# Kernel optimization log

Measured on AMD Instinct MI355X. Metric: run time of the kernel, lower is better.

## Reference

```python
import jax, jax.numpy as jnp
import numpy as np

EPS = 1e-6

def _layernorm(x, gamma, beta):
    mu = jnp.mean(x, axis=-1, keepdims=True)
    var = jnp.mean(jnp.square(x - mu), axis=-1, keepdims=True)
    return (x - mu) * jax.lax.rsqrt(var + EPS) * gamma + beta


def setup_inputs() -> dict:
    key = jax.random.key(0)
    ks = jax.random.split(key, 8)
    B, N, C, F = 2, 2048, 1024, 4096
    s = 0.02
    return {
        "x": jax.random.normal(ks[0], (B, N, C), jnp.float32),
        "Wq": jax.random.normal(ks[1], (C, C), jnp.float32) * s,
        "Wk": jax.random.normal(ks[2], (C, C), jnp.float32) * s,
        "Wv": jax.random.normal(ks[3], (C, C), jnp.float32) * s,
        "Wp": jax.random.normal(ks[4], (C, C), jnp.float32) * s,
        "bp": jnp.zeros((C,), jnp.float32),
        "W1": jax.random.normal(ks[5], (C, F), jnp.float32) * s,
        "b1": jnp.zeros((F,), jnp.float32),
        "W2": jax.random.normal(ks[6], (F, C), jnp.float32) * s,
        "b2": jnp.zeros((C,), jnp.float32),
        "gamma1": jnp.ones((C,), jnp.float32),
        "beta1": jnp.zeros((C,), jnp.float32),
        "gamma2": jnp.ones((C,), jnp.float32),
        "beta2": jnp.zeros((C,), jnp.float32),
    }


def reference(x, Wq, Wk, Wv, Wp, bp, W1, b1, W2, b2, gamma1, beta1, gamma2, beta2):
    B, N, C = x.shape
    H = 16
    D = C // H
    scale = D ** -0.5

    xn = _layernorm(x, gamma1, beta1)
    # QKV projections (no bias); q pre-scaled by head_dim**-0.5 as in source
    q = (xn @ Wq * scale).reshape(B, N, H, D).transpose(0, 2, 1, 3)  # bhnd
    k = (xn @ Wk).reshape(B, N, H, D).transpose(0, 2, 1, 3)
    v = (xn @ Wv).reshape(B, N, H, D).transpose(0, 2, 1, 3)

    attn = jax.nn.softmax(jnp.einsum("bhnd,bhmd->bhnm", q, k), axis=-1)
    y = jnp.einsum("bhnm,bhmd->bhnd", attn, v)
    y = y.transpose(0, 2, 1, 3).reshape(B, N, C)
    x = x + (y @ Wp + bp)

    xn2 = _layernorm(x, gamma2, beta2)
    h = jax.nn.gelu(xn2 @ W1 + b1, approximate=False)  # keras 'gelu' is exact
    x = x + (h @ W2 + b2)
    return x
```

## Files before the change

### kernel.cpp

```cpp
#include <hip/hip_runtime.h>
#include <math.h>

#define BN  4096
#define SEQ 2048
#define CH  1024
#define FF  4096
#define NH  16
#define HD  64

typedef short bf16x8 __attribute__((ext_vector_type(8)));
typedef float f32x4  __attribute__((ext_vector_type(4)));

#define MFMA16(a,b,c) __builtin_amdgcn_mfma_f32_16x16x32_bf16(a,b,c,0,0,0)

__device__ __forceinline__ unsigned short f2b(float f){
  unsigned u = __float_as_uint(f);
  u += 0x7fffu + ((u>>16)&1u);
  return (unsigned short)(u>>16);
}

__device__ __forceinline__ unsigned pk2(float a, float b){
  return __builtin_amdgcn_perm(__float_as_uint(b), __float_as_uint(a), 0x07060302u);
}

#if __has_builtin(__builtin_amdgcn_exp2f)
__device__ __forceinline__ float fexp2(float x){ return __builtin_amdgcn_exp2f(x); }
#else
__device__ __forceinline__ float fexp2(float x){
  float r; asm("v_exp_f32 %0, %1" : "=v"(r) : "v"(x)); return r;
}
#endif

__device__ __forceinline__ void gl2lds16(const void* g, void* l){
  __builtin_amdgcn_global_load_lds(
      (__attribute__((address_space(1))) void*)g,
      (__attribute__((address_space(3))) void*)l, 16, 0, 0);
}

__global__ __launch_bounds__(256) void transpose_all(
    const float* __restrict__ Wq, const float* __restrict__ Wk,
    const float* __restrict__ Wv, const float* __restrict__ Wp,
    const float* __restrict__ W1, const float* __restrict__ W2,
    unsigned short* __restrict__ wq_t, unsigned short* __restrict__ wk_t,
    unsigned short* __restrict__ wv_t, unsigned short* __restrict__ wp_t,
    unsigned short* __restrict__ w1_t, unsigned short* __restrict__ w2_t)
{
  const int id = blockIdx.x;
  const float* in; unsigned short* out; int R, S, bx, by; float scale = 1.f;
  if (id < 1024){
    const int which = id >> 8, sub = id & 255;
    R = CH; S = CH; bx = sub & 15; by = sub >> 4;
    if (which == 0){ in = Wq; out = wq_t; scale = 0.18033688011112042f; }
    else if (which == 1){ in = Wk; out = wk_t; }
    else if (which == 2){ in = Wv; out = wv_t; }
    else               { in = Wp; out = wp_t; }
  } else if (id < 2048){
    const int sub = id - 1024; in = W1; out = w1_t; R = CH; S = FF;
    bx = sub & 63; by = sub >> 6;
  } else {
    const int sub = id - 2048; in = W2; out = w2_t; R = FF; S = CH;
    bx = sub & 15; by = sub >> 4;
  }
  __shared__ float tile[64][65];
  const int tid = threadIdx.x;
  const int tx = tid & 63, ty = tid >> 6;
  const int s0 = bx * 64, r0 = by * 64;
  #pragma unroll
  for (int j = 0; j < 16; j++){
    int r = ty + j*4;
    tile[r][tx] = in[(size_t)(r0 + r)*S + s0 + tx];
  }
  __syncthreads();
  #pragma unroll
  for (int j = 0; j < 16; j++){
    int s = ty + j*4;
    out[(size_t)(s0 + s)*R + r0 + tx] = f2b(tile[tx][s] * scale);
  }
}

__global__ __launch_bounds__(256) void ln_kernel(const float* __restrict__ x,
    const float* __restrict__ gamma, const float* __restrict__ beta,
    unsigned short* __restrict__ out)
{
  const int row = blockIdx.x, tid = threadIdx.x;
  const float4 xv = ((const float4*)(x + (size_t)row*CH))[tid];
  float s  = xv.x + xv.y + xv.z + xv.w;
  float ss = xv.x*xv.x + xv.y*xv.y + xv.z*xv.z + xv.w*xv.w;
  #pragma unroll
  for (int off = 1; off < 64; off <<= 1){
    s  += __shfl_xor(s,  off, 64);
    ss += __shfl_xor(ss, off, 64);
  }
  __shared__ float red[8];
  const int w = tid >> 6;
  if ((tid & 63) == 0){ red[w] = s; red[4+w] = ss; }
  __syncthreads();
  s  = red[0]+red[1]+red[2]+red[3];
  ss = red[4]+red[5]+red[6]+red[7];
  const float mu   = s * (1.f/CH);
  const float rstd = rsqrtf(ss*(1.f/CH) - mu*mu + 1e-6f);
  const float4 g = ((const float4*)gamma)[tid];
  const float4 b = ((const float4*)beta )[tid];
  ushort4 o;
  o.x = f2b((xv.x-mu)*rstd*g.x + b.x);
  o.y = f2b((xv.y-mu)*rstd*g.y + b.y);
  o.z = f2b((xv.z-mu)*rstd*g.z + b.z);
  o.w = f2b((xv.w-mu)*rstd*g.w + b.w);
  ((ushort4*)(out + (size_t)row*CH))[tid] = o;
}

template<int BNT,int BIAS,int GELU,int RES,int OMODE,int SPLITK>
__global__ __launch_bounds__(256,2) void gemm_bt(const unsigned short* __restrict__ A,
    const unsigned short* __restrict__ Bt, const float* __restrict__ bias,
    const float* __restrict__ resid, float* __restrict__ outF,
    unsigned short* __restrict__ outB, unsigned short* __restrict__ outK,
    unsigned short* __restrict__ outV, int M, int Nn, int K)
{
  constexpr int MI = (BNT==128) ? 4 : 2;
  constexpr int BCH = (BNT==128) ? 4 : 2;
  __shared__ __align__(16) unsigned short Al[128*64];
  __shared__ __align__(16) unsigned short Bl[BNT*64];
  const int tid = threadIdx.x;
  const int w = tid >> 6, lane = tid & 63;
  const int quad = lane >> 4, l16 = lane & 15;
  const int m0 = blockIdx.y*128, n0 = blockIdx.x*BNT;
  const int wm = (BNT==128) ? (w >> 1)*64 : w*32;
  const int wn = (BNT==128) ? (w & 1)*64 : 0;
  const int srow = lane >> 3, sslot = lane & 7;
  f32x4 acc[MI][4] = {};
  const int kseg = SPLITK > 1 ? K / SPLITK : K;
  const int kBeg = SPLITK > 1 ? blockIdx.z * kseg : 0;
  for (int k0 = kBeg; k0 < kBeg + kseg; k0 += 64){
    __syncthreads();
    #pragma unroll
    for (int i = 0; i < 4; i++){
      const int rb = (w*4 + i)*8;
      const int r = rb + srow;
      const int c = sslot ^ (r & 7);
      gl2lds16(A + (size_t)(m0 + r)*K + k0 + c*8, (char*)Al + rb*128);
    }
    #pragma unroll
    for (int i = 0; i < BCH; i++){
      const int rb = (w*BCH + i)*8;
      const int r = rb + srow;
      const int c = sslot ^ (r & 7);
      gl2lds16(Bt + (size_t)(n0 + r)*K + k0 + c*8, (char*)Bl + rb*128);
    }
    __syncthreads();
    #pragma unroll
    for (int kc = 0; kc < 2; kc++){
      bf16x8 af[MI], bfr[4];
      #pragma unroll
      for (int mi = 0; mi < MI; mi++){
        const int r = wm + mi*16 + l16;
        af[mi] = *(const bf16x8*)(Al + r*64 + (((kc*4 + quad) ^ (r & 7))*8));
      }
      #pragma unroll
      for (int nj = 0; nj < 4; nj++){
        const int r = wn + nj*16 + l16;
        bfr[nj] = *(const bf16x8*)(Bl + r*64 + (((kc*4 + quad) ^ (r & 7))*8));
      }
      #pragma unroll
      for (int mi = 0; mi < MI; mi++)
        #pragma unroll
        for (int nj = 0; nj < 4; nj++)
          acc[mi][nj] = MFMA16(af[mi], bfr[nj], acc[mi][nj]);
    }
  }
  #pragma unroll
  for (int nj = 0; nj < 4; nj++){
    const int col = n0 + wn + nj*16 + l16;
    const float bv = BIAS ? bias[col] : 0.f;
    #pragma unroll
    for (int mi = 0; mi < MI; mi++){
      #pragma unroll
      for (int r = 0; r < 4; r++){
        const int row = m0 + wm + mi*16 + quad*4 + r;
        float v = acc[mi][nj][r];
        if (SPLITK > 1){
          if (blockIdx.z == 0){
            if (BIAS) v += bias[col];
            if (RES)  v += resid[(size_t)row*Nn + col];
          }
          atomicAdd(&outF[(size_t)row*Nn + col], v);
          continue;
        }
        v += bv;
        if (GELU) v = 0.5f*v*(1.f + erff(v*0.70710678118654752f));
        if (RES)  v += resid[(size_t)row*Nn + col];
        if (OMODE == 0) outF[(size_t)row*Nn + col] = v;
        else if (OMODE == 1) outB[(size_t)row*Nn + col] = f2b(v);
        else {
          const int cg = col >> 10, c = col & (CH-1);
          if (cg == 0)      outB[(size_t)row*CH + c] = f2b(v);
          else if (cg == 1) outK[(size_t)row*CH + c] = f2b(v);
          else {
            const int bb = row >> 11, n = row & (SEQ-1);
            const int hh = c >> 6,  d = c & (HD-1);
            const int np = (n & ~63) | (((n & 15) << 2) | ((n >> 4) & 3));
            outV[((size_t)((bb*NH + hh)*HD + d))*SEQ + np] = f2b(v);
          }
        }
      }
    }
  }
}

__global__ __launch_bounds__(256,2) void attn_kernel(const unsigned short* __restrict__ q,
    const unsigned short* __restrict__ k, const unsigned short* __restrict__ vt,
    unsigned short* __restrict__ y)
{
  __shared__ __align__(16) unsigned short Kl[2][64*64];
  __shared__ __align__(16) unsigned short Vl[2][64*64];
  __shared__ __align__(16) unsigned short Pp[4][64*68];
  const int tid = threadIdx.x;
  const int w = tid >> 6, lane = tid & 63;
  const int wq = w & 1, wk = w >> 1;
  const int quad = lane >> 4, l16 = lane & 15;
  const int bh = blockIdx.y;
  const int b = bh >> 4, h = bh & 15;
  const size_t tb  = ((size_t)b*SEQ)*CH + h*HD;
  const size_t vb_ = (size_t)bh*HD*SEQ;
  const int qr0 = blockIdx.x*128 + wq*64;

  bf16x8 qf[4][2];
  #pragma unroll
  for (int mi = 0; mi < 4; mi++)
    #pragma unroll
    for (int kc = 0; kc < 2; kc++)
      qf[mi][kc] = *(const bf16x8*)(q + tb + (size_t)(qr0 + mi*16 + l16)*CH + kc*32 + quad*8);

  float sacc[4][4];
  f32x4 o[4][4] = {};
  #pragma unroll
  for (int mi = 0; mi < 4; mi++)
    #pragma unroll
    for (int r = 0; r < 4; r++) sacc[mi][r] = 0.f;

  for (int t = 0; t < 16; t++){
    const int kv0 = wk*1024 + t*64;
    __syncthreads();
    #pragma unroll
    for (int i = 0; i < 8; i++){
      const int r = i*8 + (lane >> 3);
      const int c = (lane & 7) ^ (r & 7);
      if (wq == 0)
        gl2lds16(k  + tb  + (size_t)(kv0 + r)*CH + c*8, (char*)&Kl[wk][0] + i*1024);
      else
        gl2lds16(vt + vb_ + (size_t)r*SEQ + kv0 + c*8, (char*)&Vl[wk][0] + i*1024);
    }
    __syncthreads();

    f32x4 s[4][4] = {};
    #pragma unroll
    for (int kc = 0; kc < 2; kc++){
      #pragma unroll
      for (int nj = 0; nj < 4; nj++){
        bf16x8 kf = *(const bf16x8*)(&Kl[wk][0] + (nj*16 + l16)*64 + (((kc*4 + quad) ^ (l16 & 7))*8));
        #pragma unroll
        for (int mi = 0; mi < 4; mi++)
          s[mi][nj] = MFMA16(qf[mi][kc], kf, s[mi][nj]);
      }
    }
    #pragma unroll
    for (int mi = 0; mi < 4; mi++){
      #pragma unroll
      for (int r = 0; r < 4; r++){
        const float p0 = fexp2(s[mi][0][r]);
        const float p1 = fexp2(s[mi][1][r]);
        const float p2 = fexp2(s[mi][2][r]);
        const float p3 = fexp2(s[mi][3][r]);
        sacc[mi][r] += (p0 + p1) + (p2 + p3);
        uint2 pk;
        pk.x = pk2(p0, p1);
        pk.y = pk2(p2, p3);
        const int prow = mi*16 + quad*4 + r;
        *(uint2*)(&Pp[w][prow*68 + l16*4]) = pk;
      }
    }
    #pragma unroll
    for (int kc = 0; kc < 2; kc++){
      bf16x8 pa[4];
      #pragma unroll
      for (int mi = 0; mi < 4; mi++)
        pa[mi] = *(const bf16x8*)(&Pp[w][(mi*16 + l16)*68 + kc*32 + quad*8]);
      #pragma unroll
      for (int nd = 0; nd < 4; nd++){
        bf16x8 vf = *(const bf16x8*)(&Vl[wk][0] + (nd*16 + l16)*64 + (((kc*4 + quad) ^ (l16 & 7))*8));
        #pragma unroll
        for (int mi = 0; mi < 4; mi++)
          o[mi][nd] = MFMA16(pa[mi], vf, o[mi][nd]);
      }
    }
  }

  __syncthreads();
  float* ob = wq ? (float*)&Vl[0][0] : (float*)&Kl[0][0];
  float* sb = (float*)&Pp[2 + wq][0];
  if (wk == 1){
    #pragma unroll
    for (int mi = 0; mi < 4; mi++)
      #pragma unroll
      for (int nd = 0; nd < 4; nd++)
        #pragma unroll
        for (int r = 0; r < 4; r++){
          const int idx = (mi*4 + nd)*4 + r;
          ob[lane*64 + ((idx + lane) & 63)] = o[mi][nd][r];
        }
    #pragma unroll
    for (int mi = 0; mi < 4; mi++)
      #pragma unroll
      for (int r = 0; r < 4; r++)
        sb[lane*16 + ((mi*4 + r + lane) & 15)] = sacc[mi][r];
  }
  __syncthreads();
  if (wk == 0){
    #pragma unroll
    for (int mi = 0; mi < 4; mi++)
      #pragma unroll
      for (int nd = 0; nd < 4; nd++)
        #pragma unroll
        for (int r = 0; r < 4; r++){
          const int idx = (mi*4 + nd)*4 + r;
          o[mi][nd][r] += ob[lane*64 + ((idx + lane) & 63)];
        }
    #pragma unroll
    for (int mi = 0; mi < 4; mi++){
      #pragma unroll
      for (int r = 0; r < 4; r++){
        float sum = sacc[mi][r] + sb[lane*16 + ((mi*4 + r + lane) & 15)];
        #pragma unroll
        for (int off = 1; off < 16; off <<= 1) sum += __shfl_xor(sum, off, 64);
        const float inv = 1.f / sum;
        const int qr = qr0 + mi*16 + quad*4 + r;
        #pragma unroll
        for (int nd = 0; nd < 4; nd++)
          y[tb + (size_t)qr*CH + nd*16 + l16] = f2b(o[mi][nd][r]*inv);
      }
    }
  }
}

extern "C" void kernel_launch(void* const* d_in, const int* in_sizes, int n_in,
                              void* d_out, int out_size, void* d_ws, size_t ws_size,
                              hipStream_t stream)
{
  (void)in_sizes; (void)n_in; (void)out_size; (void)ws_size;
  const float* x   = (const float*)d_in[0];
  const float* Wq  = (const float*)d_in[1];
  const float* Wk  = (const float*)d_in[2];
  const float* Wv  = (const float*)d_in[3];
  const float* Wp  = (const float*)d_in[4];
  const float* bp  = (const float*)d_in[5];
  const float* W1  = (const float*)d_in[6];
  const float* b1  = (const float*)d_in[7];
  const float* W2  = (const float*)d_in[8];
  const float* b2  = (const float*)d_in[9];
  const float* g1  = (const float*)d_in[10];
  const float* be1 = (const float*)d_in[11];
  const float* g2  = (const float*)d_in[12];
  const float* be2 = (const float*)d_in[13];
  float* out = (float*)d_out;
  char* ws = (char*)d_ws;
  const size_t MB = 1024*1024;
  unsigned short* wq_t = (unsigned short*)(ws +  0*MB);
  unsigned short* wk_t = (unsigned short*)(ws +  2*MB);
  unsigned short* wv_t = (unsigned short*)(ws +  4*MB);
  unsigned short* wp_t = (unsigned short*)(ws +  6*MB);
  unsigned short* w1_t = (unsigned short*)(ws +  8*MB);
  unsigned short* w2_t = (unsigned short*)(ws + 16*MB);
  unsigned short* xn   = (unsigned short*)(ws + 24*MB);
  unsigned short* qb   = (unsigned short*)(ws + 32*MB);
  unsigned short* kb   = (unsigned short*)(ws + 40*MB);
  unsigned short* vtb  = (unsigned short*)(ws + 48*MB);
  unsigned short* yb   = (unsigned short*)(ws + 56*MB);
  float*          x2   = (float*)         (ws + 64*MB);
  unsigned short* xn2  = (unsigned short*)(ws + 80*MB);
  unsigned short* hb   = (unsigned short*)(ws + 88*MB);

  transpose_all<<<3072,256,0,stream>>>(Wq, Wk, Wv, Wp, W1, W2,
                                       wq_t, wk_t, wv_t, wp_t, w1_t, w2_t);

  ln_kernel<<<BN,256,0,stream>>>(x, g1, be1, xn);
  gemm_bt<128,0,0,0,3,0><<<dim3(24,32),256,0,stream>>>(xn, wq_t, nullptr, nullptr,
      nullptr, qb, kb, vtb, BN, 3072, CH);
  attn_kernel<<<dim3(16,32),256,0,stream>>>(qb, kb, vtb, yb);
  gemm_bt<64,1,0,1,0,0><<<dim3(16,32),256,0,stream>>>(yb, wp_t, bp, x, x2,
      nullptr, nullptr, nullptr, BN, CH, CH);
  ln_kernel<<<BN,256,0,stream>>>(x2, g2, be2, xn2);
  gemm_bt<128,1,1,0,1,0><<<dim3(32,32),256,0,stream>>>(xn2, w1_t, b1, nullptr, nullptr,
      hb, nullptr, nullptr, BN, FF, CH);
  hipMemsetAsync(out, 0, (size_t)BN*CH*sizeof(float), stream);
  gemm_bt<128,1,0,1,0,4><<<dim3(8,32,4),256,0,stream>>>(hb, w2_t, b2, x2, out,
      nullptr, nullptr, nullptr, BN, CH, FF);
}
```

Before: 381.1 us.

## Fuse LayerNorm into weight-prep kernel, shrink attention P buffer, retune W2 GEMM

```diff
diff --git a/kernel.cpp b/kernel.cpp
--- a/kernel.cpp
+++ b/kernel.cpp
@@ -37,7 +37,9 @@
       (__attribute__((address_space(3))) void*)l, 16, 0, 0);
 }
 
-__global__ __launch_bounds__(256) void transpose_all(
+__global__ __launch_bounds__(256) void prep_kernel(
+    const float* __restrict__ x, const float* __restrict__ g1,
+    const float* __restrict__ be1, unsigned short* __restrict__ xn,
     const float* __restrict__ Wq, const float* __restrict__ Wk,
     const float* __restrict__ Wv, const float* __restrict__ Wp,
     const float* __restrict__ W1, const float* __restrict__ W2,
@@ -46,6 +48,35 @@
     unsigned short* __restrict__ w1_t, unsigned short* __restrict__ w2_t)
 {
   const int id = blockIdx.x;
+  const int tid = threadIdx.x;
+  if (id >= 3072){
+    const int row = id - 3072;
+    const float4 xv = ((const float4*)(x + (size_t)row*CH))[tid];
+    float s  = xv.x + xv.y + xv.z + xv.w;
+    float ss = xv.x*xv.x + xv.y*xv.y + xv.z*xv.z + xv.w*xv.w;
+    #pragma unroll
+    for (int off = 1; off < 64; off <<= 1){
+      s  += __shfl_xor(s,  off, 64);
+      ss += __shfl_xor(ss, off, 64);
+    }
+    __shared__ float red[8];
+    const int w = tid >> 6;
+    if ((tid & 63) == 0){ red[w] = s; red[4+w] = ss; }
+    __syncthreads();
+    s  = red[0]+red[1]+red[2]+red[3];
+    ss = red[4]+red[5]+red[6]+red[7];
+    const float mu   = s * (1.f/CH);
+    const float rstd = rsqrtf(ss*(1.f/CH) - mu*mu + 1e-6f);
+    const float4 g = ((const float4*)g1)[tid];
+    const float4 b = ((const float4*)be1)[tid];
+    ushort4 o;
+    o.x = f2b((xv.x-mu)*rstd*g.x + b.x);
+    o.y = f2b((xv.y-mu)*rstd*g.y + b.y);
+    o.z = f2b((xv.z-mu)*rstd*g.z + b.z);
+    o.w = f2b((xv.w-mu)*rstd*g.w + b.w);
+    ((ushort4*)(xn + (size_t)row*CH))[tid] = o;
+    return;
+  }
   const float* in; unsigned short* out; int R, S, bx, by; float scale = 1.f;
   if (id < 1024){
     const int which = id >> 8, sub = id & 255;
@@ -62,7 +93,6 @@
     bx = sub & 15; by = sub >> 4;
   }
   __shared__ float tile[64][65];
-  const int tid = threadIdx.x;
   const int tx = tid & 63, ty = tid >> 6;
   const int s0 = bx * 64, r0 = by * 64;
   #pragma unroll
@@ -206,17 +236,19 @@
   }
 }
 
-__global__ __launch_bounds__(256,2) void attn_kernel(const unsigned short* __restrict__ q,
+__global__ __launch_bounds__(256,3) void attn_kernel(const unsigned short* __restrict__ q,
     const unsigned short* __restrict__ k, const unsigned short* __restrict__ vt,
     unsigned short* __restrict__ y)
 {
   __shared__ __align__(16) unsigned short Kl[2][64*64];
   __shared__ __align__(16) unsigned short Vl[2][64*64];
-  __shared__ __align__(16) unsigned short Pp[4][64*68];
+  __shared__ __align__(16) unsigned short Pp[4][64*40];
   const int tid = threadIdx.x;
   const int w = tid >> 6, lane = tid & 63;
   const int wq = w & 1, wk = w >> 1;
   const int quad = lane >> 4, l16 = lane & 15;
+  const int phalf = l16 >> 3;
+  const int l8 = l16 & 7;
   const int bh = blockIdx.y;
   const int b = bh >> 4, h = bh & 15;
   const size_t tb  = ((size_t)b*SEQ)*CH + h*HD;
@@ -262,6 +294,7 @@
           s[mi][nj] = MFMA16(qf[mi][kc], kf, s[mi][nj]);
       }
     }
+    uint2 stash[4][4];
     #pragma unroll
     for (int mi = 0; mi < 4; mi++){
       #pragma unroll
@@ -275,15 +308,25 @@
         pk.x = pk2(p0, p1);
         pk.y = pk2(p2, p3);
         const int prow = mi*16 + quad*4 + r;
-        *(uint2*)(&Pp[w][prow*68 + l16*4]) = pk;
+        if (phalf == 0) *(uint2*)(&Pp[w][prow*40 + l8*4]) = pk;
+        else            stash[mi][r] = pk;
       }
     }
     #pragma unroll
     for (int kc = 0; kc < 2; kc++){
+      if (kc == 1){
+        if (phalf == 1){
+          #pragma unroll
+          for (int mi = 0; mi < 4; mi++)
+            #pragma unroll
+            for (int r = 0; r < 4; r++)
+              *(uint2*)(&Pp[w][(mi*16 + quad*4 + r)*40 + l8*4]) = stash[mi][r];
+        }
+      }
       bf16x8 pa[4];
       #pragma unroll
       for (int mi = 0; mi < 4; mi++)
-        pa[mi] = *(const bf16x8*)(&Pp[w][(mi*16 + l16)*68 + kc*32 + quad*8]);
+        pa[mi] = *(const bf16x8*)(&Pp[w][(mi*16 + l16)*40 + quad*8]);
       #pragma unroll
       for (int nd = 0; nd < 4; nd++){
         bf16x8 vf = *(const bf16x8*)(&Vl[wk][0] + (nd*16 + l16)*64 + (((kc*4 + quad) ^ (l16 & 7))*8));
@@ -378,10 +421,9 @@
   unsigned short* xn2  = (unsigned short*)(ws + 80*MB);
   unsigned short* hb   = (unsigned short*)(ws + 88*MB);
 
-  transpose_all<<<3072,256,0,stream>>>(Wq, Wk, Wv, Wp, W1, W2,
-                                       wq_t, wk_t, wv_t, wp_t, w1_t, w2_t);
-
-  ln_kernel<<<BN,256,0,stream>>>(x, g1, be1, xn);
+  prep_kernel<<<7168,256,0,stream>>>(x, g1, be1, xn,
+      Wq, Wk, Wv, Wp, W1, W2, wq_t, wk_t, wv_t, wp_t, w1_t, w2_t);
+
   gemm_bt<128,0,0,0,3,0><<<dim3(24,32),256,0,stream>>>(xn, wq_t, nullptr, nullptr,
       nullptr, qb, kb, vtb, BN, 3072, CH);
   attn_kernel<<<dim3(16,32),256,0,stream>>>(qb, kb, vtb, yb);
@@ -391,6 +433,6 @@
   gemm_bt<128,1,1,0,1,0><<<dim3(32,32),256,0,stream>>>(xn2, w1_t, b1, nullptr, nullptr,
       hb, nullptr, nullptr, BN, FF, CH);
   hipMemsetAsync(out, 0, (size_t)BN*CH*sizeof(float), stream);
-  gemm_bt<128,1,0,1,0,4><<<dim3(8,32,4),256,0,stream>>>(hb, w2_t, b2, x2, out,
+  gemm_bt<64,1,0,1,0,2><<<dim3(16,32,2),256,0,stream>>>(hb, w2_t, b2, x2, out,
       nullptr, nullptr, nullptr, BN, CH, FF);
 }
```

Measured after the change: 695.9 us. +82.6%, slower.
